# Kernel optimization log

Measured on AMD Instinct MI355X. Metric: run time of the kernel, lower is better.

## Reference

```python
import jax, jax.numpy as jnp
import numpy as np

B, N, DIM = 4, 2048, 1024
HEADS, DHEAD = 16, 64
N_MEM = 64
INNER = HEADS * DHEAD  # 1024


def setup_inputs() -> dict:
    key = jax.random.key(0)
    ks = jax.random.split(key, 8)
    x = jax.random.normal(ks[0], (B, N, DIM), dtype=jnp.float32)
    memories = jax.random.normal(ks[1], (N_MEM, DIM), dtype=jnp.float32)
    attn_mask = jnp.ones((1, 1, N, N + N_MEM), dtype=bool)
    scale = 1.0 / np.sqrt(DIM)
    ln_gamma = jnp.ones((DIM,), dtype=jnp.float32)
    ln_beta = jnp.zeros((DIM,), dtype=jnp.float32)
    Wq = jax.random.normal(ks[2], (DIM, INNER), dtype=jnp.float32) * scale
    Wkv = jax.random.normal(ks[3], (DIM, 2 * INNER), dtype=jnp.float32) * scale
    Wo = jax.random.normal(ks[4], (INNER, DIM), dtype=jnp.float32) * scale
    bo = jnp.zeros((DIM,), dtype=jnp.float32)
    return {"x": x, "attn_mask": attn_mask, "memories": memories,
            "ln_gamma": ln_gamma, "ln_beta": ln_beta,
            "Wq": Wq, "Wkv": Wkv, "Wo": Wo, "bo": bo}


def _layernorm(x, gamma, beta, eps=1e-5):
    mu = jnp.mean(x, axis=-1, keepdims=True)
    var = jnp.var(x, axis=-1, keepdims=True)
    return (x - mu) * jax.lax.rsqrt(var + eps) * gamma + beta


def reference(x, attn_mask, memories, ln_gamma, ln_beta, Wq, Wkv, Wo, bo):
    b = x.shape[0]
    xn = _layernorm(x, ln_gamma, ln_beta)
    # memories: [n_mem, d] -> broadcast to [b, n_mem, d], concat on kv length
    mem = jnp.broadcast_to(memories[None], (b, memories.shape[0], memories.shape[1]))
    x_kv = jnp.concatenate([xn, mem], axis=1)  # [b, n+n_mem, d]
    q = xn @ Wq                                 # [b, n, inner]
    kv = x_kv @ Wkv                             # [b, nk, 2*inner]
    k, v = jnp.split(kv, 2, axis=-1)
    # split heads: b n (h d) -> b h n d
    def heads(t):
        bsz, n, _ = t.shape
        return t.reshape(bsz, n, HEADS, DHEAD).transpose(0, 2, 1, 3)
    q, k, v = heads(q), heads(k), heads(v)
    scale = DHEAD ** -0.5
    dots = jnp.einsum('bhnd,bhmd->bhnm', q, k) * scale  # [b,h,n,nk]
    neg = -jnp.finfo(dots.dtype).max
    dots = jnp.where(attn_mask, dots, neg)
    attn = jax.nn.softmax(dots, axis=-1)
    out = jnp.einsum('bhnm,bhmd->bhnd', attn, v)        # [b,h,n,d]
    out = out.transpose(0, 2, 1, 3).reshape(b, -1, INNER)
    return out @ Wo + bo
```

## Files before the change

kernel.cpp:

```cpp
#include <hip/hip_runtime.h>

using f16 = _Float16;
typedef _Float16 f16x8 __attribute__((ext_vector_type(8)));
typedef _Float16 f16x4 __attribute__((ext_vector_type(4)));
typedef float f32x4 __attribute__((ext_vector_type(4)));
typedef float f32x16 __attribute__((ext_vector_type(16)));
typedef uint32_t u32;
typedef unsigned int u32x4 __attribute__((ext_vector_type(4)));
typedef __fp16 h16x2 __attribute__((ext_vector_type(2)));

constexpr int DIMC   = 1024;
constexpr int NSEQ   = 2048;
constexpr int NKV    = 2112;
constexpr int NCHUNK = 33;
constexpr int NBATCH = 4;

__device__ __forceinline__ int swz8(int row, int slot) { return slot ^ (row & 7); }

__device__ __forceinline__ u32 pkrtz(float a, float b) {
    h16x2 t = __builtin_amdgcn_cvt_pkrtz(a, b);
    return __builtin_bit_cast(u32, t);
}

__device__ __forceinline__ void gld16(const f16* g, f16* l) {
    __builtin_amdgcn_global_load_lds(
        (const __attribute__((address_space(1))) u32*)g,
        (__attribute__((address_space(3))) u32*)l,
        16, 0, 0);
}

__global__ __launch_bounds__(256)
void ln_kernel(const float* __restrict__ x, const float* __restrict__ gamma,
               const float* __restrict__ beta, f16* __restrict__ xn)
{
    const int row = blockIdx.x;
    const int tid = threadIdx.x;
    const float4 v = *reinterpret_cast<const float4*>(x + (size_t)row * DIMC + tid * 4);
    float s  = v.x + v.y + v.z + v.w;
    float ss = v.x*v.x + v.y*v.y + v.z*v.z + v.w*v.w;
#pragma unroll
    for (int off = 1; off < 64; off <<= 1) {
        s  += __shfl_xor(s,  off, 64);
        ss += __shfl_xor(ss, off, 64);
    }
    __shared__ float ps[4], pss[4];
    const int w = tid >> 6;
    if ((tid & 63) == 0) { ps[w] = s; pss[w] = ss; }
    __syncthreads();
    s  = ps[0]  + ps[1]  + ps[2]  + ps[3];
    ss = pss[0] + pss[1] + pss[2] + pss[3];
    const float mu   = s * (1.0f / 1024.0f);
    const float var  = ss * (1.0f / 1024.0f) - mu * mu;
    const float rstd = rsqrtf(var + 1e-5f);
    const float4 gv = *reinterpret_cast<const float4*>(gamma + tid * 4);
    const float4 bv = *reinterpret_cast<const float4*>(beta  + tid * 4);
    f16x4 o;
    o[0] = (f16)((v.x - mu) * rstd * gv.x + bv.x);
    o[1] = (f16)((v.y - mu) * rstd * gv.y + bv.y);
    o[2] = (f16)((v.z - mu) * rstd * gv.z + bv.z);
    o[3] = (f16)((v.w - mu) * rstd * gv.w + bv.w);
    *reinterpret_cast<f16x4*>(xn + (size_t)row * DIMC + tid * 4) = o;
}

__device__ __forceinline__ void transpose_tile(
    const float* __restrict__ in, f16* __restrict__ out,
    int R, int C, float scale, int bx, int by)
{
    __shared__ float tile[32][33];
    const int c0 = bx * 32;
    const int r0 = by * 32;
    const int tx = threadIdx.x;
    const int ty = threadIdx.y;
#pragma unroll
    for (int i = 0; i < 4; ++i)
        tile[ty + i * 8][tx] = in[(size_t)(r0 + ty + i * 8) * C + c0 + tx];
    __syncthreads();
#pragma unroll
    for (int i = 0; i < 4; ++i)
        out[(size_t)(c0 + ty + i * 8) * R + r0 + tx] = (f16)(tile[tx][ty + i * 8] * scale);
}

__global__ __launch_bounds__(256)
void prep_kernel(const float* __restrict__ Wq, const float* __restrict__ Wkv,
                 const float* __restrict__ Wo, const float* __restrict__ mem,
                 f16* __restrict__ wqT, f16* __restrict__ wkvT,
                 f16* __restrict__ woT, f16* __restrict__ mem16)
{
    const int bx = blockIdx.x, by = blockIdx.y;
    if (by < 32) {
        if (bx < 32) transpose_tile(Wq, wqT, 1024, 1024, 0.125f * 1.44269504088896341f, bx, by);
    } else if (by < 64) {
        transpose_tile(Wkv, wkvT, 1024, 2048, 1.0f, bx, by - 32);
    } else if (by < 96) {
        if (bx < 32) transpose_tile(Wo, woT, 1024, 1024, 1.0f, bx, by - 64);
    } else {
        const int tid = threadIdx.y * 32 + threadIdx.x;
        const int i = bx * 256 + tid;
        const float4 v = *reinterpret_cast<const float4*>(mem + (size_t)i * 4);
        f16x4 o; o[0] = (f16)v.x; o[1] = (f16)v.y; o[2] = (f16)v.z; o[3] = (f16)v.w;
        *reinterpret_cast<f16x4*>(mem16 + (size_t)i * 4) = o;
    }
}

template<int MODE>
__device__ __forceinline__ void gemm_body(
    int tm, int tn, f16* As, f16* Bs,
    const f16* __restrict__ A, const f16* __restrict__ BT,
    const f16* __restrict__ mem16,
    f16* __restrict__ Cf16, f16* __restrict__ Vt,
    float* __restrict__ Cf32, const float* __restrict__ bias)
{
    const int tid = threadIdx.x;
    const int lane = tid & 63, w = tid >> 6;
    const int wm = (w >> 1) * 64, wn = (w & 1) * 64;
    const int l3 = lane >> 3, l7 = lane & 7;
    const int gslot = (l7 ^ l3) * 8;

    f32x4 acc[4][4] = {};

    const f16* ag[4];
    const f16* bg[4];
#pragma unroll
    for (int i = 0; i < 4; ++i) {
        const int rl = w * 32 + i * 8 + l3;
        const int gm = tm * 128 + rl;
        if (MODE == 1) {
            const int bb = gm / NKV;
            const int rr = gm - bb * NKV;
            ag[i] = ((rr < NSEQ) ? (A + ((size_t)bb * NSEQ + rr) * DIMC)
                                 : (mem16 + (size_t)(rr - NSEQ) * DIMC)) + gslot;
        } else {
            ag[i] = A + (size_t)gm * DIMC + gslot;
        }
        bg[i] = BT + (size_t)(tn * 128 + rl) * DIMC + gslot;
    }

    for (int kt = 0; kt < DIMC; kt += 64) {
#pragma unroll
        for (int i = 0; i < 4; ++i) {
            gld16(ag[i] + kt, &As[(w * 32 + i * 8) * 64]);
            gld16(bg[i] + kt, &Bs[(w * 32 + i * 8) * 64]);
        }
        asm volatile("s_waitcnt vmcnt(0)" ::: "memory");
        __syncthreads();
#pragma unroll
        for (int kk = 0; kk < 2; ++kk) {
            f16x8 af[4], bf[4];
            const int rsel  = lane & 15;
            const int slot0 = (lane >> 4) + kk * 4;
#pragma unroll
            for (int mi = 0; mi < 4; ++mi) {
                const int row = wm + mi * 16 + rsel;
                af[mi] = *reinterpret_cast<const f16x8*>(&As[row * 64 + swz8(row, slot0) * 8]);
            }
#pragma unroll
            for (int nj = 0; nj < 4; ++nj) {
                const int row = wn + nj * 16 + rsel;
                bf[nj] = *reinterpret_cast<const f16x8*>(&Bs[row * 64 + swz8(row, slot0) * 8]);
            }
            __builtin_amdgcn_s_setprio(1);
#pragma unroll
            for (int mi = 0; mi < 4; ++mi)
#pragma unroll
                for (int nj = 0; nj < 4; ++nj)
                    acc[mi][nj] = __builtin_amdgcn_mfma_f32_16x16x32_f16(af[mi], bf[nj], acc[mi][nj], 0, 0, 0);
            __builtin_amdgcn_s_setprio(0);
        }
        __syncthreads();
    }

    const int cl = lane & 15, g = lane >> 4;
#pragma unroll
    for (int mi = 0; mi < 4; ++mi) {
#pragma unroll
        for (int nj = 0; nj < 4; ++nj) {
            const int col = tn * 128 + wn + nj * 16 + cl;
            if (MODE == 1 && col >= DIMC) {
                const int gm0 = tm * 128 + wm + mi * 16 + g * 4;
                const int bb = gm0 / NKV;
                const int rr = gm0 - bb * NKV;
                const int vc = col - DIMC;
                f16x4 pk;
                pk[0] = (f16)acc[mi][nj][0]; pk[1] = (f16)acc[mi][nj][1];
                pk[2] = (f16)acc[mi][nj][2]; pk[3] = (f16)acc[mi][nj][3];
                *reinterpret_cast<f16x4*>(
                    Vt + ((((size_t)bb * 16 + (vc >> 6)) * NCHUNK + (rr >> 6)) * 64 + (vc & 63)) * 64 + (rr & 63)) = pk;
            } else {
#pragma unroll
                for (int j = 0; j < 4; ++j) {
                    const int gm = tm * 128 + wm + mi * 16 + g * 4 + j;
                    const float val = acc[mi][nj][j];
                    if (MODE == 0) {
                        const int bb = gm >> 11, rr = gm & 2047;
                        Cf16[(((size_t)bb * 16 + (col >> 6)) * NSEQ + rr) * 64 + (col & 63)] = (f16)val;
                    } else if (MODE == 1) {
                        const int bb = gm / NKV;
                        const int rr = gm - bb * NKV;
                        Cf16[(((size_t)bb * 16 + (col >> 6)) * NKV + rr) * 64 + (col & 63)] = (f16)val;
                    } else {
                        Cf32[(size_t)gm * DIMC + col] = val + bias[col];
                    }
                }
            }
        }
    }
}

__global__ __launch_bounds__(256, 3)
void gemm_qkv(const f16* __restrict__ xn, const f16* __restrict__ wqT,
              const f16* __restrict__ wkvT, const f16* __restrict__ mem16,
              f16* __restrict__ q16, f16* __restrict__ k16, f16* __restrict__ vt16)
{
    __shared__ __align__(16) f16 As[128 * 64];
    __shared__ __align__(16) f16 Bs[128 * 64];
    if (blockIdx.y < 16) {
        gemm_body<1>(blockIdx.x, blockIdx.y, As, Bs, xn, wkvT, mem16, k16, vt16, nullptr, nullptr);
    } else {
        if (blockIdx.x >= 64) return;
        gemm_body<0>(blockIdx.x, blockIdx.y - 16, As, Bs, xn, wqT, nullptr, q16, nullptr, nullptr, nullptr);
    }
}

__global__ __launch_bounds__(256, 3)
void gemm_o(const f16* __restrict__ ao, const f16* __restrict__ woT,
            float* __restrict__ out, const float* __restrict__ bo)
{
    __shared__ __align__(16) f16 As[128 * 64];
    __shared__ __align__(16) f16 Bs[128 * 64];
    gemm_body<2>(blockIdx.x, blockIdx.y, As, Bs, ao, woT, nullptr, nullptr, nullptr, out, bo);
}

__global__ __launch_bounds__(512, 4)
void attn_kernel(const f16* __restrict__ q16, const f16* __restrict__ k16,
                 const f16* __restrict__ vt16, f16* __restrict__ ao16)
{
    __shared__ __align__(16) f16 Kb[3][64 * 64];
    __shared__ __align__(16) f16 Vb[3][64 * 64];

    const int raw = blockIdx.x;
    const int bh = (raw & 7) * 8 + ((raw >> 3) & 7);
    const int qt = raw >> 6;
    const int b = bh >> 4, h = bh & 15;
    const int tid = threadIdx.x, lane = tid & 63, w = tid >> 6;
    const int l31 = lane & 31, hi = lane >> 5;
    const int l3 = lane >> 3, l7 = lane & 7;
    const int gslot = (l7 ^ l3) * 8;

    const f16* kbase = k16  + (size_t)bh * NKV * 64;
    const f16* vbase = vt16 + (size_t)bh * NCHUNK * 4096;
    const f16* qbase = q16  + (size_t)bh * NSEQ * 64;

    const int srow = w * 8 + l3;
    const f16* kp = kbase + (size_t)srow * 64 + gslot;
    const f16* vp = vbase + (size_t)srow * 64 + gslot;

    f16x8 qf[4];
    {
        const int qrow = qt * 256 + w * 32 + l31;
#pragma unroll
        for (int ks = 0; ks < 4; ++ks)
            qf[ks] = *reinterpret_cast<const f16x8*>(
                qbase + (size_t)qrow * 64 + ks * 16 + hi * 8);
    }

    f32x16 Oa0 = {}, Oa1 = {};
    float lp0 = 0.0f, lp1 = 0.0f, lp2 = 0.0f, lp3 = 0.0f;

    f32x16 minus8;
#pragma unroll
    for (int r = 0; r < 16; ++r) minus8[r] = -8.0f;

#pragma unroll
    for (int c = 0; c < 2; ++c) {
        gld16(kp + (size_t)c * 4096, &Kb[c][w * 8 * 64]);
        gld16(vp + (size_t)c * 4096, &Vb[c][w * 8 * 64]);
    }

#if __has_builtin(__builtin_amdgcn_fdot2)
    const h16x2 ones = {(__fp16)1.0f, (__fp16)1.0f};
#endif

    int cur = 0, nxt = 2;
    for (int t = 0; t < NCHUNK; ++t) {
        if (t < NCHUNK - 1) asm volatile("s_waitcnt vmcnt(2)" ::: "memory");
        else                asm volatile("s_waitcnt vmcnt(0)" ::: "memory");
        __builtin_amdgcn_s_barrier();

        if (t + 2 < NCHUNK) {
            gld16(kp + (size_t)(t + 2) * 4096, &Kb[nxt][w * 8 * 64]);
            gld16(vp + (size_t)(t + 2) * 4096, &Vb[nxt][w * 8 * 64]);
        }
        const f16* Ks = Kb[cur];
        const f16* Vs = Vb[cur];

#pragma unroll
        for (int kb = 0; kb < 2; ++kb) {
            const int krow = kb * 32 + l31;
            f16x8 kf[4];
#pragma unroll
            for (int ks = 0; ks < 4; ++ks)
                kf[ks] = *reinterpret_cast<const f16x8*>(
                    &Ks[krow * 64 + ((2 * ks + hi) ^ (krow & 7)) * 8]);

            f32x16 sA;
            __builtin_amdgcn_s_setprio(1);
            sA = __builtin_amdgcn_mfma_f32_32x32x16_f16(kf[0], qf[0], minus8, 0, 0, 0);
#pragma unroll
            for (int ks = 1; ks < 4; ++ks)
                sA = __builtin_amdgcn_mfma_f32_32x32x16_f16(kf[ks], qf[ks], sA, 0, 0, 0);
            __builtin_amdgcn_s_setprio(0);

            float p[16];
#pragma unroll
            for (int r = 0; r < 16; ++r)
                p[r] = __builtin_amdgcn_exp2f(sA[r]);

            f16x8 pb[2];
#pragma unroll
            for (int s2 = 0; s2 < 2; ++s2) {
                u32 a  = pkrtz(p[s2 * 8 + 0], p[s2 * 8 + 1]);
                u32 b2 = pkrtz(p[s2 * 8 + 2], p[s2 * 8 + 3]);
                u32 c  = pkrtz(p[s2 * 8 + 4], p[s2 * 8 + 5]);
                u32 d  = pkrtz(p[s2 * 8 + 6], p[s2 * 8 + 7]);
                asm volatile("v_permlane32_swap_b32 %0, %1" : "+v"(a),  "+v"(c));
                asm volatile("v_permlane32_swap_b32 %0, %1" : "+v"(b2), "+v"(d));
#if __has_builtin(__builtin_amdgcn_fdot2)
                lp0 = __builtin_amdgcn_fdot2(__builtin_bit_cast(h16x2, a),  ones, lp0, false);
                lp1 = __builtin_amdgcn_fdot2(__builtin_bit_cast(h16x2, b2), ones, lp1, false);
                lp2 = __builtin_amdgcn_fdot2(__builtin_bit_cast(h16x2, c),  ones, lp2, false);
                lp3 = __builtin_amdgcn_fdot2(__builtin_bit_cast(h16x2, d),  ones, lp3, false);
#else
                {
                    h16x2 ha = __builtin_bit_cast(h16x2, a),  hb = __builtin_bit_cast(h16x2, b2);
                    h16x2 hc = __builtin_bit_cast(h16x2, c),  hd = __builtin_bit_cast(h16x2, d);
                    lp0 += (float)ha[0] + (float)ha[1];
                    lp1 += (float)hb[0] + (float)hb[1];
                    lp2 += (float)hc[0] + (float)hc[1];
                    lp3 += (float)hd[0] + (float)hd[1];
                }
#endif
                u32x4 wv = {a, b2, c, d};
                pb[s2] = __builtin_bit_cast(f16x8, wv);
            }

#pragma unroll
            for (int s2 = 0; s2 < 2; ++s2) {
                const int s = kb * 2 + s2;
                const int vr1 = 32 + l31;
                const f16x8 vf0 = *reinterpret_cast<const f16x8*>(
                    &Vs[l31 * 64 + ((2 * s + hi) ^ (l31 & 7)) * 8]);
                const f16x8 vf1 = *reinterpret_cast<const f16x8*>(
                    &Vs[vr1 * 64 + ((2 * s + hi) ^ (vr1 & 7)) * 8]);
                __builtin_amdgcn_s_setprio(1);
                Oa0 = __builtin_amdgcn_mfma_f32_32x32x16_f16(vf0, pb[s2], Oa0, 0, 0, 0);
                Oa1 = __builtin_amdgcn_mfma_f32_32x32x16_f16(vf1, pb[s2], Oa1, 0, 0, 0);
                __builtin_amdgcn_s_setprio(0);
            }
        }
        cur = (cur == 2) ? 0 : cur + 1;
        nxt = (nxt == 2) ? 0 : nxt + 1;
    }

    float l0 = (lp0 + lp1) + (lp2 + lp3);
    l0 += __shfl_xor(l0, 32, 64);
    const float rinv = 1.0f / l0;
    const int qrow = qt * 256 + w * 32 + l31;
#pragma unroll
    for (int rq = 0; rq < 4; ++rq) {
        const int d0 = rq * 8 + hi * 4;
        f16x4 pk;
        pk[0] = (f16)(Oa0[rq * 4 + 0] * rinv);
        pk[1] = (f16)(Oa0[rq * 4 + 1] * rinv);
        pk[2] = (f16)(Oa0[rq * 4 + 2] * rinv);
        pk[3] = (f16)(Oa0[rq * 4 + 3] * rinv);
        *reinterpret_cast<f16x4*>(
            ao16 + ((size_t)(b * NSEQ + qrow)) * DIMC + h * 64 + d0) = pk;
    }
#pragma unroll
    for (int rq = 0; rq < 4; ++rq) {
        const int d0 = 32 + rq * 8 + hi * 4;
        f16x4 pk;
        pk[0] = (f16)(Oa1[rq * 4 + 0] * rinv);
        pk[1] = (f16)(Oa1[rq * 4 + 1] * rinv);
        pk[2] = (f16)(Oa1[rq * 4 + 2] * rinv);
        pk[3] = (f16)(Oa1[rq * 4 + 3] * rinv);
        *reinterpret_cast<f16x4*>(
            ao16 + ((size_t)(b * NSEQ + qrow)) * DIMC + h * 64 + d0) = pk;
    }
}

extern "C" void kernel_launch(void* const* d_in, const int* in_sizes, int n_in,
                              void* d_out, int out_size, void* d_ws, size_t ws_size,
                              hipStream_t stream)
{
    const float* x        = (const float*)d_in[0];
    const float* memories = (const float*)d_in[2];
    const float* ln_gamma = (const float*)d_in[3];
    const float* ln_beta  = (const float*)d_in[4];
    const float* Wq       = (const float*)d_in[5];
    const float* Wkv      = (const float*)d_in[6];
    const float* Wo       = (const float*)d_in[7];
    const float* bo       = (const float*)d_in[8];
    float* out = (float*)d_out;

    char* ws = (char*)d_ws;
    f16* xn16  = (f16*)(ws);
    f16* q16   = (f16*)(ws + (16ull << 20));
    f16* k16   = (f16*)(ws + (32ull << 20));
    f16* vt16  = (f16*)(ws + (49ull << 20));
    f16* wqT   = (f16*)(ws + (66ull << 20));
    f16* wkvT  = (f16*)(ws + (68ull << 20));
    f16* woT   = (f16*)(ws + (72ull << 20));
    f16* mem16 = (f16*)(ws + (74ull << 20));
    f16* ao16  = xn16;

    prep_kernel<<<dim3(64, 97), dim3(32, 8), 0, stream>>>(
        Wq, Wkv, Wo, memories, wqT, wkvT, woT, mem16);

    ln_kernel<<<NBATCH * NSEQ, 256, 0, stream>>>(x, ln_gamma, ln_beta, xn16);

    gemm_qkv<<<dim3(66, 24), 256, 0, stream>>>(xn16, wqT, wkvT, mem16, q16, k16, vt16);

    attn_kernel<<<dim3(512), 512, 0, stream>>>(q16, k16, vt16, ao16);

    gemm_o<<<dim3(64, 8), 256, 0, stream>>>(ao16, woT, out, bo);

    (void)in_sizes; (void)n_in; (void)out_size; (void)ws_size;
}
```

Baseline: 196.0 us.

## Replace QKV GEMM with 256x256 tiled, double-buffered pipelined kernel

The QKV projection GEMM moves from 128x128 tiles with 256 threads to 256x256 tiles with 512 threads (8 waves). The LDS buffers are double-buffered, and the next K-tile's global loads are interleaved with MFMA work using partial vmcnt waits and raw s_barrier. This is meant to raise data reuse per loaded byte and hide global load latency behind compute. The trade-off is a large LDS footprint (128KB) and high register use, which limits occupancy to one block per CU. The old 128-tile body is kept only for the output GEMM, trimmed to the MODE 2 epilogue.

```diff
diff --git a/kernel.cpp b/kernel.cpp
--- a/kernel.cpp
+++ b/kernel.cpp
@@ -103,80 +103,129 @@
 }
 
 template<int MODE>
-__device__ __forceinline__ void gemm_body(
-    int tm, int tn, f16* As, f16* Bs,
+__device__ __forceinline__ void gemm256_body(
+    int tm, int tn, f16* Lds,
     const f16* __restrict__ A, const f16* __restrict__ BT,
     const f16* __restrict__ mem16,
     f16* __restrict__ Cf16, f16* __restrict__ Vt,
     float* __restrict__ Cf32, const float* __restrict__ bias)
 {
+    constexpr int NK = 16;
     const int tid = threadIdx.x;
     const int lane = tid & 63, w = tid >> 6;
-    const int wm = (w >> 1) * 64, wn = (w & 1) * 64;
-    const int l3 = lane >> 3, l7 = lane & 7;
-    const int gslot = (l7 ^ l3) * 8;
-
-    f32x4 acc[4][4] = {};
-
-    const f16* ag[4];
-    const f16* bg[4];
-#pragma unroll
-    for (int i = 0; i < 4; ++i) {
-        const int rl = w * 32 + i * 8 + l3;
-        const int gm = tm * 128 + rl;
-        if (MODE == 1) {
-            const int bb = gm / NKV;
-            const int rr = gm - bb * NKV;
-            ag[i] = ((rr < NSEQ) ? (A + ((size_t)bb * NSEQ + rr) * DIMC)
-                                 : (mem16 + (size_t)(rr - NSEQ) * DIMC)) + gslot;
-        } else {
-            ag[i] = A + (size_t)gm * DIMC + gslot;
-        }
-        bg[i] = BT + (size_t)(tn * 128 + rl) * DIMC + gslot;
-    }
-
-    for (int kt = 0; kt < DIMC; kt += 64) {
-#pragma unroll
-        for (int i = 0; i < 4; ++i) {
-            gld16(ag[i] + kt, &As[(w * 32 + i * 8) * 64]);
-            gld16(bg[i] + kt, &Bs[(w * 32 + i * 8) * 64]);
-        }
-        asm volatile("s_waitcnt vmcnt(0)" ::: "memory");
-        __syncthreads();
-#pragma unroll
-        for (int kk = 0; kk < 2; ++kk) {
-            f16x8 af[4], bf[4];
-            const int rsel  = lane & 15;
-            const int slot0 = (lane >> 4) + kk * 4;
-#pragma unroll
-            for (int mi = 0; mi < 4; ++mi) {
-                const int row = wm + mi * 16 + rsel;
-                af[mi] = *reinterpret_cast<const f16x8*>(&As[row * 64 + swz8(row, slot0) * 8]);
-            }
-#pragma unroll
-            for (int nj = 0; nj < 4; ++nj) {
-                const int row = wn + nj * 16 + rsel;
-                bf[nj] = *reinterpret_cast<const f16x8*>(&Bs[row * 64 + swz8(row, slot0) * 8]);
-            }
+    const int wmh = w >> 2;
+    const int wnq = w & 3;
+    const int rsel = lane & 15, g = lane >> 4;
+    const int t3 = tid >> 3;
+    const int gslot = ((tid & 7) ^ (t3 & 7)) * 8;
+
+#define AHp(slot, h) (Lds + (((slot)*2 + 0)*2 + (h)) * 8192)
+#define BHp(slot, h) (Lds + (((slot)*2 + 1)*2 + (h)) * 8192)
+
+    const f16* ag[2][2];
+    const f16* bg[2][2];
+#pragma unroll
+    for (int h = 0; h < 2; ++h)
+#pragma unroll
+        for (int s = 0; s < 2; ++s) {
+            const int rl = h * 128 + s * 64 + t3;
+            const int gm = tm * 256 + rl;
+            if (MODE == 1) {
+                const int bb = gm / NKV;
+                const int rr = gm - bb * NKV;
+                ag[h][s] = ((rr < NSEQ) ? (A + ((size_t)bb * NSEQ + rr) * DIMC)
+                                        : (mem16 + (size_t)(rr - NSEQ) * DIMC)) + gslot;
+            } else {
+                ag[h][s] = A + (size_t)gm * DIMC + gslot;
+            }
+            bg[h][s] = BT + (size_t)(tn * 256 + rl) * DIMC + gslot;
+        }
+
+    f32x4 acc[8][4] = {};
+
+    auto stageA2 = [&](int slot, int kt) {
+        const int kb = kt * 64;
+#pragma unroll
+        for (int h = 0; h < 2; ++h) {
+            gld16(ag[h][0] + kb, AHp(slot, h) + (w * 8) * 64);
+            gld16(ag[h][1] + kb, AHp(slot, h) + (64 + w * 8) * 64);
+        }
+    };
+    auto stageB1 = [&](int slot, int kt, int h) {
+        const int kb = kt * 64;
+        gld16(bg[h][0] + kb, BHp(slot, h) + (w * 8) * 64);
+        gld16(bg[h][1] + kb, BHp(slot, h) + (64 + w * 8) * 64);
+    };
+
+    stageA2(0, 0);
+    stageB1(0, 0, 0); stageB1(0, 0, 1);
+    stageB1(1, 1, 0); stageB1(1, 1, 1);
+    asm volatile("s_waitcnt vmcnt(4)" ::: "memory");
+    asm volatile("s_barrier" ::: "memory");
+
+    for (int m = 0; m < NK; ++m) {
+        const int slot = m & 1;
+        const f16* Ah = AHp(slot, wmh);
+        const f16* Bh = BHp(slot, wnq >> 1);
+        const int brow0 = (wnq & 1) * 64;
+
+        f16x8 bf[4][2];
+#pragma unroll
+        for (int q = 0; q < 4; ++q) {
+            if (q == 0) {
+#pragma unroll
+                for (int nj = 0; nj < 4; ++nj)
+#pragma unroll
+                    for (int ks = 0; ks < 2; ++ks) {
+                        const int row = brow0 + nj * 16 + rsel;
+                        bf[nj][ks] = *reinterpret_cast<const f16x8*>(
+                            &Bh[row * 64 + ((g + ks * 4) ^ (row & 7)) * 8]);
+                    }
+            }
+            f16x8 af[2][2];
+#pragma unroll
+            for (int mi = 0; mi < 2; ++mi)
+#pragma unroll
+                for (int ks = 0; ks < 2; ++ks) {
+                    const int row = q * 32 + mi * 16 + rsel;
+                    af[mi][ks] = *reinterpret_cast<const f16x8*>(
+                        &Ah[row * 64 + ((g + ks * 4) ^ (row & 7)) * 8]);
+                }
+            if (q == 0 && m + 1 < NK) stageA2(slot ^ 1, m + 1);
+            if (q == 1 && m + 2 < NK) stageB1(slot, m + 2, 0);
+            if (q == 2 && m + 2 < NK) stageB1(slot, m + 2, 1);
+
+            asm volatile("s_barrier" ::: "memory");
+            asm volatile("s_waitcnt lgkmcnt(0)" ::: "memory");
             __builtin_amdgcn_s_setprio(1);
 #pragma unroll
-            for (int mi = 0; mi < 4; ++mi)
-#pragma unroll
-                for (int nj = 0; nj < 4; ++nj)
-                    acc[mi][nj] = __builtin_amdgcn_mfma_f32_16x16x32_f16(af[mi], bf[nj], acc[mi][nj], 0, 0, 0);
+            for (int ks = 0; ks < 2; ++ks)
+#pragma unroll
+                for (int mi = 0; mi < 2; ++mi)
+#pragma unroll
+                    for (int nj = 0; nj < 4; ++nj)
+                        acc[q * 2 + mi][nj] = __builtin_amdgcn_mfma_f32_16x16x32_f16(
+                            af[mi][ks], bf[nj][ks], acc[q * 2 + mi][nj], 0, 0, 0);
             __builtin_amdgcn_s_setprio(0);
-        }
-        __syncthreads();
-    }
-
-    const int cl = lane & 15, g = lane >> 4;
-#pragma unroll
-    for (int mi = 0; mi < 4; ++mi) {
+            if (q == 3) {
+                if (m + 2 < NK) asm volatile("s_waitcnt vmcnt(4)" ::: "memory");
+                else            asm volatile("s_waitcnt vmcnt(0)" ::: "memory");
+            }
+            asm volatile("s_barrier" ::: "memory");
+        }
+    }
+#undef AHp
+#undef BHp
+
+    const int cl = lane & 15;
+    const int wm = wmh * 128, wn = wnq * 64;
+#pragma unroll
+    for (int mi = 0; mi < 8; ++mi) {
 #pragma unroll
         for (int nj = 0; nj < 4; ++nj) {
-            const int col = tn * 128 + wn + nj * 16 + cl;
+            const int col = tn * 256 + wn + nj * 16 + cl;
             if (MODE == 1 && col >= DIMC) {
-                const int gm0 = tm * 128 + wm + mi * 16 + g * 4;
+                const int gm0 = tm * 256 + wm + mi * 16 + g * 4;
                 const int bb = gm0 / NKV;
                 const int rr = gm0 - bb * NKV;
                 const int vc = col - DIMC;
@@ -188,7 +237,7 @@
             } else {
 #pragma unroll
                 for (int j = 0; j < 4; ++j) {
-                    const int gm = tm * 128 + wm + mi * 16 + g * 4 + j;
+                    const int gm = tm * 256 + wm + mi * 16 + g * 4 + j;
                     const float val = acc[mi][nj][j];
                     if (MODE == 0) {
                         const int bb = gm >> 11, rr = gm & 2047;
@@ -206,18 +255,102 @@
     }
 }
 
-__global__ __launch_bounds__(256, 3)
-void gemm_qkv(const f16* __restrict__ xn, const f16* __restrict__ wqT,
-              const f16* __restrict__ wkvT, const f16* __restrict__ mem16,
-              f16* __restrict__ q16, f16* __restrict__ k16, f16* __restrict__ vt16)
-{
-    __shared__ __align__(16) f16 As[128 * 64];
-    __shared__ __align__(16) f16 Bs[128 * 64];
-    if (blockIdx.y < 16) {
-        gemm_body<1>(blockIdx.x, blockIdx.y, As, Bs, xn, wkvT, mem16, k16, vt16, nullptr, nullptr);
+__global__ __launch_bounds__(512, 2)
+void gemm_qkv256(const f16* __restrict__ xn, const f16* __restrict__ wqT,
+                 const f16* __restrict__ wkvT, const f16* __restrict__ mem16,
+                 f16* __restrict__ q16, f16* __restrict__ k16, f16* __restrict__ vt16)
+{
+    __shared__ __align__(16) f16 L[2 * 2 * 2 * 8192];
+    if (blockIdx.y < 8) {
+        gemm256_body<1>(blockIdx.x, blockIdx.y, L, xn, wkvT, mem16, k16, vt16, nullptr, nullptr);
     } else {
-        if (blockIdx.x >= 64) return;
-        gemm_body<0>(blockIdx.x, blockIdx.y - 16, As, Bs, xn, wqT, nullptr, q16, nullptr, nullptr, nullptr);
+        if (blockIdx.x >= 32) return;
+        gemm256_body<0>(blockIdx.x, blockIdx.y - 8, L, xn, wqT, nullptr, q16, nullptr, nullptr, nullptr);
+    }
+}
+
+template<int MODE>
+__device__ __forceinline__ void gemm_body(
+    int tm, int tn, f16* As, f16* Bs,
+    const f16* __restrict__ A, const f16* __restrict__ BT,
+    const f16* __restrict__ mem16,
+    f16* __restrict__ Cf16, f16* __restrict__ Vt,
+    float* __restrict__ Cf32, const float* __restrict__ bias)
+{
+    const int tid = threadIdx.x;
+    const int lane = tid & 63, w = tid >> 6;
+    const int wm = (w >> 1) * 64, wn = (w & 1) * 64;
+    const int l3 = lane >> 3, l7 = lane & 7;
+    const int gslot = (l7 ^ l3) * 8;
+
+    f32x4 acc[4][4] = {};
+
+    const f16* ag[4];
+    const f16* bg[4];
+#pragma unroll
+    for (int i = 0; i < 4; ++i) {
+        const int rl = w * 32 + i * 8 + l3;
+        const int gm = tm * 128 + rl;
+        if (MODE == 1) {
+            const int bb = gm / NKV;
+            const int rr = gm - bb * NKV;
+            ag[i] = ((rr < NSEQ) ? (A + ((size_t)bb * NSEQ + rr) * DIMC)
+                                 : (mem16 + (size_t)(rr - NSEQ) * DIMC)) + gslot;
+        } else {
+            ag[i] = A + (size_t)gm * DIMC + gslot;
+        }
+        bg[i] = BT + (size_t)(tn * 128 + rl) * DIMC + gslot;
+    }
+
+    for (int kt = 0; kt < DIMC; kt += 64) {
+#pragma unroll
+        for (int i = 0; i < 4; ++i) {
+            gld16(ag[i] + kt, &As[(w * 32 + i * 8) * 64]);
+            gld16(bg[i] + kt, &Bs[(w * 32 + i * 8) * 64]);
+        }
+        asm volatile("s_waitcnt vmcnt(0)" ::: "memory");
+        __syncthreads();
+#pragma unroll
+        for (int kk = 0; kk < 2; ++kk) {
+            f16x8 af[4], bf[4];
+            const int rsel  = lane & 15;
+            const int slot0 = (lane >> 4) + kk * 4;
+#pragma unroll
+            for (int mi = 0; mi < 4; ++mi) {
+                const int row = wm + mi * 16 + rsel;
+                af[mi] = *reinterpret_cast<const f16x8*>(&As[row * 64 + swz8(row, slot0) * 8]);
+            }
+#pragma unroll
+            for (int nj = 0; nj < 4; ++nj) {
+                const int row = wn + nj * 16 + rsel;
+                bf[nj] = *reinterpret_cast<const f16x8*>(&Bs[row * 64 + swz8(row, slot0) * 8]);
+            }
+            __builtin_amdgcn_s_setprio(1);
+#pragma unroll
+            for (int mi = 0; mi < 4; ++mi)
+#pragma unroll
+                for (int nj = 0; nj < 4; ++nj)
+                    acc[mi][nj] = __builtin_amdgcn_mfma_f32_16x16x32_f16(af[mi], bf[nj], acc[mi][nj], 0, 0, 0);
+            __builtin_amdgcn_s_setprio(0);
+        }
+        __syncthreads();
+    }
+
+    const int cl = lane & 15, g = lane >> 4;
+#pragma unroll
+    for (int mi = 0; mi < 4; ++mi) {
+#pragma unroll
+        for (int nj = 0; nj < 4; ++nj) {
+            const int col = tn * 128 + wn + nj * 16 + cl;
+#pragma unroll
+            for (int j = 0; j < 4; ++j) {
+                const int gm = tm * 128 + wm + mi * 16 + g * 4 + j;
+                const float val = acc[mi][nj][j];
+                if (MODE == 2) {
+                    Cf32[(size_t)gm * DIMC + col] = val + bias[col];
+                }
+            }
+        }
     }
 }
 
@@ -419,7 +552,7 @@
 
     ln_kernel<<<NBATCH * NSEQ, 256, 0, stream>>>(x, ln_gamma, ln_beta, xn16);
 
-    gemm_qkv<<<dim3(66, 24), 256, 0, stream>>>(xn16, wqT, wkvT, mem16, q16, k16, vt16);
+    gemm_qkv256<<<dim3(33, 12), 512, 0, stream>>>(xn16, wqT, wkvT, mem16, q16, k16, vt16);
 
     attn_kernel<<<dim3(512), 512, 0, stream>>>(q16, k16, vt16, ao16);
 
```

Result: no change. 195.7 us (-0.2%).

## Double-buffer GEMM shared-memory tiles to overlap global loads with MFMA

Applied to the files above, without the earlier changes.

Switches the QKV and output-projection GEMM main loop to a two-stage shared-memory ring. The next K-tile is issued before computing the current one, with a partial vmcnt wait and raw s_barrier in place of a full drain and __syncthreads. This is meant to hide global-to-LDS load latency behind MFMA work. It doubles LDS per block to 64KB and lowers the launch-bound occupancy hint from 3 to 2 blocks per CU.

```diff
diff --git a/kernel.cpp b/kernel.cpp
--- a/kernel.cpp
+++ b/kernel.cpp
@@ -135,14 +135,28 @@
         bg[i] = BT + (size_t)(tn * 128 + rl) * DIMC + gslot;
     }
 
-    for (int kt = 0; kt < DIMC; kt += 64) {
+    auto stage = [&](int kt) {
+        const int so = (kt & 1) * 8192;
+        const int kb = kt * 64;
 #pragma unroll
         for (int i = 0; i < 4; ++i) {
-            gld16(ag[i] + kt, &As[(w * 32 + i * 8) * 64]);
-            gld16(bg[i] + kt, &Bs[(w * 32 + i * 8) * 64]);
-        }
-        asm volatile("s_waitcnt vmcnt(0)" ::: "memory");
-        __syncthreads();
+            gld16(ag[i] + kb, &As[so + (w * 32 + i * 8) * 64]);
+            gld16(bg[i] + kb, &Bs[so + (w * 32 + i * 8) * 64]);
+        }
+    };
+
+    stage(0);
+    for (int kt = 0; kt < 16; ++kt) {
+        if (kt + 1 < 16) {
+            stage(kt + 1);
+            asm volatile("s_waitcnt vmcnt(8)" ::: "memory");
+        } else {
+            asm volatile("s_waitcnt vmcnt(0)" ::: "memory");
+        }
+        __builtin_amdgcn_s_barrier();
+
+        const f16* Asl = &As[(kt & 1) * 8192];
+        const f16* Bsl = &Bs[(kt & 1) * 8192];
 #pragma unroll
         for (int kk = 0; kk < 2; ++kk) {
             f16x8 af[4], bf[4];
@@ -151,12 +165,12 @@
 #pragma unroll
             for (int mi = 0; mi < 4; ++mi) {
                 const int row = wm + mi * 16 + rsel;
-                af[mi] = *reinterpret_cast<const f16x8*>(&As[row * 64 + swz8(row, slot0) * 8]);
+                af[mi] = *reinterpret_cast<const f16x8*>(&Asl[row * 64 + swz8(row, slot0) * 8]);
             }
 #pragma unroll
             for (int nj = 0; nj < 4; ++nj) {
                 const int row = wn + nj * 16 + rsel;
-                bf[nj] = *reinterpret_cast<const f16x8*>(&Bs[row * 64 + swz8(row, slot0) * 8]);
+                bf[nj] = *reinterpret_cast<const f16x8*>(&Bsl[row * 64 + swz8(row, slot0) * 8]);
             }
             __builtin_amdgcn_s_setprio(1);
 #pragma unroll
@@ -166,7 +180,7 @@
                     acc[mi][nj] = __builtin_amdgcn_mfma_f32_16x16x32_f16(af[mi], bf[nj], acc[mi][nj], 0, 0, 0);
             __builtin_amdgcn_s_setprio(0);
         }
-        __syncthreads();
+        __builtin_amdgcn_s_barrier();
     }
 
     const int cl = lane & 15, g = lane >> 4;
@@ -206,13 +220,13 @@
     }
 }
 
-__global__ __launch_bounds__(256, 3)
+__global__ __launch_bounds__(256, 2)
 void gemm_qkv(const f16* __restrict__ xn, const f16* __restrict__ wqT,
               const f16* __restrict__ wkvT, const f16* __restrict__ mem16,
               f16* __restrict__ q16, f16* __restrict__ k16, f16* __restrict__ vt16)
 {
-    __shared__ __align__(16) f16 As[128 * 64];
-    __shared__ __align__(16) f16 Bs[128 * 64];
+    __shared__ __align__(16) f16 As[2 * 128 * 64];
+    __shared__ __align__(16) f16 Bs[2 * 128 * 64];
     if (blockIdx.y < 16) {
         gemm_body<1>(blockIdx.x, blockIdx.y, As, Bs, xn, wkvT, mem16, k16, vt16, nullptr, nullptr);
     } else {
@@ -221,12 +235,12 @@
     }
 }
 
-__global__ __launch_bounds__(256, 3)
+__global__ __launch_bounds__(256, 2)
 void gemm_o(const f16* __restrict__ ao, const f16* __restrict__ woT,
             float* __restrict__ out, const float* __restrict__ bo)
 {
-    __shared__ __align__(16) f16 As[128 * 64];
-    __shared__ __align__(16) f16 Bs[128 * 64];
+    __shared__ __align__(16) f16 As[2 * 128 * 64];
+    __shared__ __align__(16) f16 Bs[2 * 128 * 64];
     gemm_body<2>(blockIdx.x, blockIdx.y, As, Bs, ao, woT, nullptr, nullptr, nullptr, out, bo);
 }
 
```

Result: slower. 202.2 us (+3.1%).
